# Kernel tuning notes

Measured on AMD Instinct MI355X. Metric: run time of the kernel, lower is better.

The kernel has to match this reference:

```python
import jax, jax.numpy as jnp
import numpy as np

NUM_HEADS = 8
Q_DIM = 32  # == k_dim == v_dim (required by the broadcasted matmul in the source)

def _conv1x1(x, w, b):
    # x: [B, C, H, W]; w: [O, C]; b: [O]  (1x1 conv == channel matmul)
    return jnp.einsum('bchw,oc->bohw', x, w) + b[None, :, None, None]

def setup_inputs() -> dict:
    key = jax.random.key(0)
    ks = jax.random.split(key, 7)
    B, C, H, W = 16, 256, 64, 64
    O = Q_DIM * NUM_HEADS  # 256
    s = 1.0 / np.sqrt(C)
    return {
        'x':  jax.random.normal(ks[0], (B, C, H, W), jnp.float32),
        'wq': jax.random.normal(ks[1], (O, C), jnp.float32) * s,
        'bq': jax.random.normal(ks[2], (O,), jnp.float32) * 0.01,
        'wk': jax.random.normal(ks[3], (O, C), jnp.float32) * s,
        'bk': jax.random.normal(ks[4], (O,), jnp.float32) * 0.01,
        'wv': jax.random.normal(ks[5], (O, C), jnp.float32) * s,
        'bv': jax.random.normal(ks[6], (O,), jnp.float32) * 0.01,
    }

def reference(x, wq, bq, wk, bk, wv, bv):
    B, C, H, W = x.shape
    nH, d = NUM_HEADS, Q_DIM
    q = _conv1x1(x, wq, bq).reshape(B, nH, d, H, W)
    k = _conv1x1(x, wk, bk).reshape(B, nH, d, H, W)
    v = _conv1x1(x, wv, bv).reshape(B, nH, d, H, W)
    # torch.matmul(q, k.transpose(-2,-1)): contract over width, batched over (B, nH, d)
    scores = jnp.einsum('bndhw,bndgw->bndhg', q, k) / jnp.sqrt(jnp.asarray(d, x.dtype))
    weights = jax.nn.softmax(scores, axis=-1)  # [B, nH, d, H, H]
    ctx = jnp.einsum('bndhg,bndgw->bndhw', weights, v)
    return ctx.reshape(B, nH * d, H, W)
```

## Files before the change

kernel.cpp:

```cpp
#include <hip/hip_runtime.h>
#include <stdint.h>

#define LOG2E       1.4426950408889634f
#define INV_SQRT32  0.17677669529663687f

using bf16x8 = __attribute__((ext_vector_type(8))) short;
using f32x4  = __attribute__((ext_vector_type(4))) float;

__device__ __forceinline__ unsigned short f2bf(float f) {
  union { float f; uint32_t u; } v; v.f = f;
  uint32_t r = v.u + 0x7fffu + ((v.u >> 16) & 1u);
  return (unsigned short)(r >> 16);
}

typedef const __attribute__((address_space(1))) void* gas_ptr;
typedef __attribute__((address_space(3))) void*       las_ptr;
__device__ __forceinline__ void load_lds16(const void* g, void* l) {
  __builtin_amdgcn_global_load_lds((gas_ptr)g, (las_ptr)l, 16, 0, 0);
}

__global__ __launch_bounds__(256) void convert_w(
    const float* __restrict__ wq, const float* __restrict__ bq,
    const float* __restrict__ wk, const float* __restrict__ bk,
    const float* __restrict__ wv, const float* __restrict__ bv,
    unsigned short* __restrict__ Wcat, float* __restrict__ biasc) {
  int idx = (blockIdx.x * 256 + threadIdx.x) * 4;
  int p = idx >> 16;
  int rem = idx & 0xffff;
  const float* src = (p == 0) ? wq : (p == 1) ? wk : wv;
  float4 v = *(const float4*)(src + rem);
  ushort4 o;
  o.x = f2bf(v.x); o.y = f2bf(v.y); o.z = f2bf(v.z); o.w = f2bf(v.w);
  *(ushort4*)(Wcat + idx) = o;
  if (blockIdx.x < 3) {
    const float* sb = (blockIdx.x == 0) ? bq : (blockIdx.x == 1) ? bk : bv;
    biasc[blockIdx.x * 256 + threadIdx.x] = sb[threadIdx.x];
  }
}

__global__ __launch_bounds__(256) void transpose_x(const float* __restrict__ x,
                                                   unsigned short* __restrict__ xt) {
  __shared__ float tile[64 * 65];
  int b = blockIdx.z;
  int s0 = blockIdx.x * 64, c0 = blockIdx.y * 64;
  int t = threadIdx.x;
  int sl = t & 63, g = t >> 6;
  const float* xp = x + ((size_t)(b * 256 + c0)) * 4096 + s0 + sl;
#pragma unroll
  for (int ii = 0; ii < 16; ++ii) {
    int cl = g * 16 + ii;
    tile[cl * 65 + sl] = xp[(size_t)cl * 4096];
  }
  __syncthreads();
#pragma unroll
  for (int it = 0; it < 2; ++it) {
    int idx = it * 256 + t;
    int s_loc = idx >> 3, cb = (idx & 7) * 8;
    unsigned short ov[8];
#pragma unroll
    for (int j = 0; j < 8; ++j) ov[j] = f2bf(tile[(cb + j) * 65 + s_loc]);
    *(uint4*)&xt[((size_t)(b * 4096 + s0 + s_loc)) * 256 + c0 + cb] = *(uint4*)ov;
  }
}

__global__ __launch_bounds__(256) void gemm_qkv(
    const unsigned short* __restrict__ Wc, const float* __restrict__ biasc,
    const unsigned short* __restrict__ Xt, unsigned short* __restrict__ qkv) {
  __shared__ unsigned short As[2][128 * 32];
  __shared__ unsigned short Bs[2][128 * 32];
  int blk = blockIdx.x;
  int b = blk / 192;
  int rest = blk - b * 192;
  int mt = rest >> 5, nt = rest & 31;
  int m0 = mt * 128, n0 = nt * 128;
  int tid = threadIdx.x;
  int lane = tid & 63, wave = tid >> 6;
  int quad = lane >> 4, rt = lane & 15;
  int wm = wave >> 1, wn = wave & 1;

  f32x4 acc[4][4];
#pragma unroll
  for (int i = 0; i < 4; ++i)
#pragma unroll
    for (int j = 0; j < 4; ++j) acc[i][j] = (f32x4){0.f, 0.f, 0.f, 0.f};

  int lr = lane >> 2;
  int sl_src = (lane & 3) ^ ((lane >> 3) & 3);
  const unsigned short* gA0 = Wc + (size_t)(m0 + wave * 32 + lr) * 256 + sl_src * 8;
  const unsigned short* gA1 = gA0 + 16 * 256;
  const unsigned short* gB0 = Xt + ((size_t)b * 4096 + n0 + wave * 32 + lr) * 256 + sl_src * 8;
  const unsigned short* gB1 = gB0 + 16 * 256;

#define STAGE(bufi, ko)                                        \
  do {                                                         \
    load_lds16(gA0 + (ko), &As[bufi][wave * 1024]);            \
    load_lds16(gA1 + (ko), &As[bufi][wave * 1024 + 512]);      \
    load_lds16(gB0 + (ko), &Bs[bufi][wave * 1024]);            \
    load_lds16(gB1 + (ko), &Bs[bufi][wave * 1024 + 512]);      \
  } while (0)

  int rsw = (quad ^ ((rt >> 1) & 3)) * 8;

  STAGE(0, 0);
  STAGE(1, 32);

#define KSTEP(kc, WAITN)                                                      \
  do {                                                                        \
    asm volatile("s_waitcnt vmcnt(" #WAITN ")" ::: "memory");                 \
    __builtin_amdgcn_s_barrier();                                             \
    __builtin_amdgcn_sched_barrier(0);                                        \
    const unsigned short* A_ = As[(kc) & 1];                                  \
    const unsigned short* B_ = Bs[(kc) & 1];                                  \
    bf16x8 af[4], bfr[4];                                                     \
    _Pragma("unroll")                                                         \
    for (int mi = 0; mi < 4; ++mi)                                            \
      af[mi] = *(const bf16x8*)&A_[(wm * 64 + mi * 16 + rt) * 32 + rsw];      \
    _Pragma("unroll")                                                         \
    for (int ni = 0; ni < 4; ++ni)                                            \
      bfr[ni] = *(const bf16x8*)&B_[(wn * 64 + ni * 16 + rt) * 32 + rsw];     \
    _Pragma("unroll")                                                         \
    for (int mi = 0; mi < 4; ++mi)                                            \
      _Pragma("unroll")                                                       \
      for (int ni = 0; ni < 4; ++ni)                                          \
        acc[mi][ni] = __builtin_amdgcn_mfma_f32_16x16x32_bf16(af[mi], bfr[ni], acc[mi][ni], 0, 0, 0); \
    __builtin_amdgcn_sched_barrier(0);                                        \
    __builtin_amdgcn_s_barrier();                                             \
    if ((kc) + 2 < 8) STAGE((kc) & 1, ((kc) + 2) * 32);                       \
  } while (0)

  KSTEP(0, 4);
  KSTEP(1, 4);
  KSTEP(2, 4);
  KSTEP(3, 4);
  KSTEP(4, 4);
  KSTEP(5, 4);
  KSTEP(6, 4);
  KSTEP(7, 0);
#undef KSTEP
#undef STAGE

  size_t obase = (size_t)b * 768;
#pragma unroll
  for (int mi = 0; mi < 4; ++mi) {
    int o = m0 + wm * 64 + mi * 16 + quad * 4;
    float bsv[4];
#pragma unroll
    for (int r = 0; r < 4; ++r) bsv[r] = biasc[o + r];
#pragma unroll
    for (int ni = 0; ni < 4; ++ni) {
      int s = n0 + wn * 64 + ni * 16 + rt;
#pragma unroll
      for (int r = 0; r < 4; ++r)
        qkv[(obase + o + r) * 4096 + s] = f2bf(acc[mi][ni][r] + bsv[r]);
    }
  }
}

__global__ __launch_bounds__(256) void attn(const unsigned short* __restrict__ qkv,
                                            float* __restrict__ out) {
  __shared__ char sh[36608];
  unsigned short* Qs = (unsigned short*)sh;
  unsigned short* Ks = (unsigned short*)(sh + 9216);
  float*          Sf = (float*)sh;
  unsigned short* Ps = (unsigned short*)(sh + 16640);
  unsigned short* Vt = (unsigned short*)(sh + 25856);
  float* red    = (float*)(sh + 35072);
  float* rowmax = (float*)(sh + 36096);
  float* rowinv = (float*)(sh + 36352);

  int blk = blockIdx.x;
  int b = blk >> 8, o = blk & 255;
  int t = threadIdx.x;
  size_t base = ((size_t)b * 768 + o) * 4096;
  const unsigned short* qg = qkv + base;
  const unsigned short* kg = qkv + base + (size_t)256 * 4096;
  const unsigned short* vg = qkv + base + (size_t)512 * 4096;

  {
    int h = t >> 2, w0 = (t & 3) * 16;
    const uint4* qp = (const uint4*)(qg + h * 64 + w0);
    const uint4* kp = (const uint4*)(kg + h * 64 + w0);
    uint4 q0 = qp[0], q1 = qp[1];
    uint4 k0 = kp[0], k1 = kp[1];
    *(uint4*)&Qs[h * 72 + w0]     = q0;
    *(uint4*)&Qs[h * 72 + w0 + 8] = q1;
    *(uint4*)&Ks[h * 72 + w0]     = k0;
    *(uint4*)&Ks[h * 72 + w0 + 8] = k1;

    int w = t & 63, gb = (t >> 6) * 16;
    unsigned short vv[16];
#pragma unroll
    for (int j = 0; j < 16; ++j) vv[j] = vg[(size_t)(gb + j) * 64 + w];
    *(uint4*)&Vt[w * 72 + gb]     = ((uint4*)vv)[0];
    *(uint4*)&Vt[w * 72 + gb + 8] = ((uint4*)vv)[1];
  }
  __syncthreads();

  int lane = t & 63, wave = t >> 6;
  int rt = lane & 15, quad = lane >> 4;
  int wm = wave >> 1, wn = wave & 1;

  f32x4 accs[2][2];
#pragma unroll
  for (int i = 0; i < 2; ++i)
#pragma unroll
    for (int j = 0; j < 2; ++j) accs[i][j] = (f32x4){0.f, 0.f, 0.f, 0.f};
#pragma unroll
  for (int ks = 0; ks < 2; ++ks) {
    int kk = ks * 32 + quad * 8;
    bf16x8 a0 = *(const bf16x8*)&Qs[(wm * 32 + rt) * 72 + kk];
    bf16x8 a1 = *(const bf16x8*)&Qs[(wm * 32 + 16 + rt) * 72 + kk];
    bf16x8 b0 = *(const bf16x8*)&Ks[(wn * 32 + rt) * 72 + kk];
    bf16x8 b1 = *(const bf16x8*)&Ks[(wn * 32 + 16 + rt) * 72 + kk];
    accs[0][0] = __builtin_amdgcn_mfma_f32_16x16x32_bf16(a0, b0, accs[0][0], 0, 0, 0);
    accs[0][1] = __builtin_amdgcn_mfma_f32_16x16x32_bf16(a0, b1, accs[0][1], 0, 0, 0);
    accs[1][0] = __builtin_amdgcn_mfma_f32_16x16x32_bf16(a1, b0, accs[1][0], 0, 0, 0);
    accs[1][1] = __builtin_amdgcn_mfma_f32_16x16x32_bf16(a1, b1, accs[1][1], 0, 0, 0);
  }
  __syncthreads();

#pragma unroll
  for (int tm = 0; tm < 2; ++tm)
#pragma unroll
    for (int tn = 0; tn < 2; ++tn)
#pragma unroll
      for (int r = 0; r < 4; ++r)
        Sf[(wm * 32 + tm * 16 + quad * 4 + r) * 65 + wn * 32 + tn * 16 + rt] =
            accs[tm][tn][r] * INV_SQRT32;
  __syncthreads();

  int hr = t & 63, qt = t >> 6;
  float s[16];
#pragma unroll
  for (int e = 0; e < 16; ++e) s[e] = Sf[hr * 65 + qt * 16 + e];
  float m = s[0];
#pragma unroll
  for (int e = 1; e < 16; ++e) m = fmaxf(m, s[e]);
  red[qt * 64 + hr] = m;
  __syncthreads();
  if (t < 64)
    rowmax[t] = fmaxf(fmaxf(red[t], red[64 + t]), fmaxf(red[128 + t], red[192 + t]));
  __syncthreads();
  float mr = rowmax[hr];
  float ssum = 0.f;
  unsigned short pv[16];
#pragma unroll
  for (int e = 0; e < 16; ++e) {
    float p = exp2f((s[e] - mr) * LOG2E);
    ssum += p;
    pv[e] = f2bf(p);
  }
  *(uint4*)&Ps[hr * 72 + qt * 16]     = ((uint4*)pv)[0];
  *(uint4*)&Ps[hr * 72 + qt * 16 + 8] = ((uint4*)pv)[1];
  red[qt * 64 + hr] = ssum;
  __syncthreads();
  if (t < 64) rowinv[t] = 1.f / (red[t] + red[64 + t] + red[128 + t] + red[192 + t]);
  __syncthreads();

  f32x4 acco[2][2];
#pragma unroll
  for (int i = 0; i < 2; ++i)
#pragma unroll
    for (int j = 0; j < 2; ++j) acco[i][j] = (f32x4){0.f, 0.f, 0.f, 0.f};
#pragma unroll
  for (int ks = 0; ks < 2; ++ks) {
    int kk = ks * 32 + quad * 8;
    bf16x8 a0 = *(const bf16x8*)&Ps[(wm * 32 + rt) * 72 + kk];
    bf16x8 a1 = *(const bf16x8*)&Ps[(wm * 32 + 16 + rt) * 72 + kk];
    bf16x8 b0 = *(const bf16x8*)&Vt[(wn * 32 + rt) * 72 + kk];
    bf16x8 b1 = *(const bf16x8*)&Vt[(wn * 32 + 16 + rt) * 72 + kk];
    acco[0][0] = __builtin_amdgcn_mfma_f32_16x16x32_bf16(a0, b0, acco[0][0], 0, 0, 0);
    acco[0][1] = __builtin_amdgcn_mfma_f32_16x16x32_bf16(a0, b1, acco[0][1], 0, 0, 0);
    acco[1][0] = __builtin_amdgcn_mfma_f32_16x16x32_bf16(a1, b0, acco[1][0], 0, 0, 0);
    acco[1][1] = __builtin_amdgcn_mfma_f32_16x16x32_bf16(a1, b1, acco[1][1], 0, 0, 0);
  }

  float* op = out + ((size_t)(b * 256 + o)) * 4096;
#pragma unroll
  for (int tm = 0; tm < 2; ++tm) {
#pragma unroll
    for (int r = 0; r < 4; ++r) {
      int h = wm * 32 + tm * 16 + quad * 4 + r;
      float inv = rowinv[h];
#pragma unroll
      for (int tn = 0; tn < 2; ++tn) {
        int w = wn * 32 + tn * 16 + rt;
        op[h * 64 + w] = acco[tm][tn][r] * inv;
      }
    }
  }
}

extern "C" void kernel_launch(void* const* d_in, const int* in_sizes, int n_in,
                              void* d_out, int out_size, void* d_ws, size_t ws_size,
                              hipStream_t stream) {
  const float* x  = (const float*)d_in[0];
  const float* wq = (const float*)d_in[1];
  const float* bq = (const float*)d_in[2];
  const float* wk = (const float*)d_in[3];
  const float* bk = (const float*)d_in[4];
  const float* wv = (const float*)d_in[5];
  const float* bv = (const float*)d_in[6];
  float* out = (float*)d_out;

  char* ws = (char*)d_ws;
  unsigned short* Wcat  = (unsigned short*)ws;
  float*          biasc = (float*)(ws + 393216);
  unsigned short* Xt    = (unsigned short*)(ws + 396288);
  unsigned short* qkv   = (unsigned short*)(ws + 396288 + 33554432);

  hipLaunchKernelGGL(convert_w, dim3(192), dim3(256), 0, stream,
                     wq, bq, wk, bk, wv, bv, Wcat, biasc);
  hipLaunchKernelGGL(transpose_x, dim3(64, 4, 16), dim3(256), 0, stream, x, Xt);
  hipLaunchKernelGGL(gemm_qkv, dim3(3072), dim3(256), 0, stream, Wcat, biasc, Xt, qkv);
  hipLaunchKernelGGL(attn, dim3(4096), dim3(256), 0, stream, qkv, out);
}
```

Baseline: 199.9 us.

## Triple-buffer GEMM, vectorize stores, register-level softmax in attention kernel

```diff
diff --git a/kernel.cpp b/kernel.cpp
--- a/kernel.cpp
+++ b/kernel.cpp
@@ -66,8 +66,8 @@
 __global__ __launch_bounds__(256) void gemm_qkv(
     const unsigned short* __restrict__ Wc, const float* __restrict__ biasc,
     const unsigned short* __restrict__ Xt, unsigned short* __restrict__ qkv) {
-  __shared__ unsigned short As[2][128 * 32];
-  __shared__ unsigned short Bs[2][128 * 32];
+  __shared__ unsigned short As[3][128 * 32];
+  __shared__ unsigned short Bs[3][128 * 32];
   int blk = blockIdx.x;
   int b = blk / 192;
   int rest = blk - b * 192;
@@ -103,14 +103,15 @@
 
   STAGE(0, 0);
   STAGE(1, 32);
+  STAGE(2, 64);
 
 #define KSTEP(kc, WAITN)                                                      \
   do {                                                                        \
     asm volatile("s_waitcnt vmcnt(" #WAITN ")" ::: "memory");                 \
     __builtin_amdgcn_s_barrier();                                             \
     __builtin_amdgcn_sched_barrier(0);                                        \
-    const unsigned short* A_ = As[(kc) & 1];                                  \
-    const unsigned short* B_ = Bs[(kc) & 1];                                  \
+    const unsigned short* A_ = As[(kc) % 3];                                  \
+    const unsigned short* B_ = Bs[(kc) % 3];                                  \
     bf16x8 af[4], bfr[4];                                                     \
     _Pragma("unroll")                                                         \
     for (int mi = 0; mi < 4; ++mi)                                            \
@@ -122,18 +123,18 @@
     for (int mi = 0; mi < 4; ++mi)                                            \
       _Pragma("unroll")                                                       \
       for (int ni = 0; ni < 4; ++ni)                                          \
-        acc[mi][ni] = __builtin_amdgcn_mfma_f32_16x16x32_bf16(af[mi], bfr[ni], acc[mi][ni], 0, 0, 0); \
+        acc[mi][ni] = __builtin_amdgcn_mfma_f32_16x16x32_bf16(bfr[ni], af[mi], acc[mi][ni], 0, 0, 0); \
     __builtin_amdgcn_sched_barrier(0);                                        \
     __builtin_amdgcn_s_barrier();                                             \
-    if ((kc) + 2 < 8) STAGE((kc) & 1, ((kc) + 2) * 32);                       \
+    if ((kc) + 3 < 8) STAGE((kc) % 3, ((kc) + 3) * 32);                       \
   } while (0)
 
-  KSTEP(0, 4);
-  KSTEP(1, 4);
-  KSTEP(2, 4);
-  KSTEP(3, 4);
-  KSTEP(4, 4);
-  KSTEP(5, 4);
+  KSTEP(0, 8);
+  KSTEP(1, 8);
+  KSTEP(2, 8);
+  KSTEP(3, 8);
+  KSTEP(4, 8);
+  KSTEP(5, 8);
   KSTEP(6, 4);
   KSTEP(7, 0);
 #undef KSTEP
@@ -142,31 +143,28 @@
   size_t obase = (size_t)b * 768;
 #pragma unroll
   for (int mi = 0; mi < 4; ++mi) {
-    int o = m0 + wm * 64 + mi * 16 + quad * 4;
-    float bsv[4];
-#pragma unroll
-    for (int r = 0; r < 4; ++r) bsv[r] = biasc[o + r];
+    int o = m0 + wm * 64 + mi * 16 + rt;
+    float bo = biasc[o];
+    size_t rowb = (obase + o) * 4096;
 #pragma unroll
     for (int ni = 0; ni < 4; ++ni) {
-      int s = n0 + wn * 64 + ni * 16 + rt;
-#pragma unroll
-      for (int r = 0; r < 4; ++r)
-        qkv[(obase + o + r) * 4096 + s] = f2bf(acc[mi][ni][r] + bsv[r]);
+      int s = n0 + wn * 64 + ni * 16 + quad * 4;
+      ushort4 st;
+      st.x = f2bf(acc[mi][ni][0] + bo);
+      st.y = f2bf(acc[mi][ni][1] + bo);
+      st.z = f2bf(acc[mi][ni][2] + bo);
+      st.w = f2bf(acc[mi][ni][3] + bo);
+      *(ushort4*)&qkv[rowb + s] = st;
     }
   }
 }
 
 __global__ __launch_bounds__(256) void attn(const unsigned short* __restrict__ qkv,
                                             float* __restrict__ out) {
-  __shared__ char sh[36608];
-  unsigned short* Qs = (unsigned short*)sh;
-  unsigned short* Ks = (unsigned short*)(sh + 9216);
-  float*          Sf = (float*)sh;
-  unsigned short* Ps = (unsigned short*)(sh + 16640);
-  unsigned short* Vt = (unsigned short*)(sh + 25856);
-  float* red    = (float*)(sh + 35072);
-  float* rowmax = (float*)(sh + 36096);
-  float* rowinv = (float*)(sh + 36352);
+  __shared__ unsigned short Vt[64 * 72];
+  __shared__ unsigned short Ps[64 * 72];
+  __shared__ float redm[128];
+  __shared__ float reds[128];
 
   int blk = blockIdx.x;
   int b = blk >> 8, o = blk & 255;
@@ -176,30 +174,15 @@
   const unsigned short* kg = qkv + base + (size_t)256 * 4096;
   const unsigned short* vg = qkv + base + (size_t)512 * 4096;
 
-  {
-    int h = t >> 2, w0 = (t & 3) * 16;
-    const uint4* qp = (const uint4*)(qg + h * 64 + w0);
-    const uint4* kp = (const uint4*)(kg + h * 64 + w0);
-    uint4 q0 = qp[0], q1 = qp[1];
-    uint4 k0 = kp[0], k1 = kp[1];
-    *(uint4*)&Qs[h * 72 + w0]     = q0;
-    *(uint4*)&Qs[h * 72 + w0 + 8] = q1;
-    *(uint4*)&Ks[h * 72 + w0]     = k0;
-    *(uint4*)&Ks[h * 72 + w0 + 8] = k1;
-
-    int w = t & 63, gb = (t >> 6) * 16;
-    unsigned short vv[16];
-#pragma unroll
-    for (int j = 0; j < 16; ++j) vv[j] = vg[(size_t)(gb + j) * 64 + w];
-    *(uint4*)&Vt[w * 72 + gb]     = ((uint4*)vv)[0];
-    *(uint4*)&Vt[w * 72 + gb + 8] = ((uint4*)vv)[1];
-  }
-  __syncthreads();
-
   int lane = t & 63, wave = t >> 6;
   int rt = lane & 15, quad = lane >> 4;
   int wm = wave >> 1, wn = wave & 1;
 
+  int vw = t & 63, gb = (t >> 6) * 16;
+  unsigned short vv[16];
+#pragma unroll
+  for (int j = 0; j < 16; ++j) vv[j] = vg[(size_t)(gb + j) * 64 + vw];
+
   f32x4 accs[2][2];
 #pragma unroll
   for (int i = 0; i < 2; ++i)
@@ -208,53 +191,82 @@
 #pragma unroll
   for (int ks = 0; ks < 2; ++ks) {
     int kk = ks * 32 + quad * 8;
-    bf16x8 a0 = *(const bf16x8*)&Qs[(wm * 32 + rt) * 72 + kk];
-    bf16x8 a1 = *(const bf16x8*)&Qs[(wm * 32 + 16 + rt) * 72 + kk];
-    bf16x8 b0 = *(const bf16x8*)&Ks[(wn * 32 + rt) * 72 + kk];
-    bf16x8 b1 = *(const bf16x8*)&Ks[(wn * 32 + 16 + rt) * 72 + kk];
+    bf16x8 a0 = *(const bf16x8*)&qg[(wm * 32 + rt) * 64 + kk];
+    bf16x8 a1 = *(const bf16x8*)&qg[(wm * 32 + 16 + rt) * 64 + kk];
+    bf16x8 b0 = *(const bf16x8*)&kg[(wn * 32 + rt) * 64 + kk];
+    bf16x8 b1 = *(const bf16x8*)&kg[(wn * 32 + 16 + rt) * 64 + kk];
     accs[0][0] = __builtin_amdgcn_mfma_f32_16x16x32_bf16(a0, b0, accs[0][0], 0, 0, 0);
     accs[0][1] = __builtin_amdgcn_mfma_f32_16x16x32_bf16(a0, b1, accs[0][1], 0, 0, 0);
     accs[1][0] = __builtin_amdgcn_mfma_f32_16x16x32_bf16(a1, b0, accs[1][0], 0, 0, 0);
     accs[1][1] = __builtin_amdgcn_mfma_f32_16x16x32_bf16(a1, b1, accs[1][1], 0, 0, 0);
   }
+
+  float sv[2][2][4];
+#pragma unroll
+  for (int tm = 0; tm < 2; ++tm)
+#pragma unroll
+    for (int tn = 0; tn < 2; ++tn)
+#pragma unroll
+      for (int r = 0; r < 4; ++r) sv[tm][tn][r] = accs[tm][tn][r] * INV_SQRT32;
+
+  float pmax[2][4];
+#pragma unroll
+  for (int tm = 0; tm < 2; ++tm)
+#pragma unroll
+    for (int r = 0; r < 4; ++r) {
+      float m = fmaxf(sv[tm][0][r], sv[tm][1][r]);
+      m = fmaxf(m, __shfl_xor(m, 1));
+      m = fmaxf(m, __shfl_xor(m, 2));
+      m = fmaxf(m, __shfl_xor(m, 4));
+      m = fmaxf(m, __shfl_xor(m, 8));
+      pmax[tm][r] = m;
+    }
+  if (rt == 0) {
+#pragma unroll
+    for (int tm = 0; tm < 2; ++tm)
+#pragma unroll
+      for (int r = 0; r < 4; ++r)
+        redm[wn * 64 + wm * 32 + tm * 16 + quad * 4 + r] = pmax[tm][r];
+  }
   __syncthreads();
 
+  float psum[2][4];
+  unsigned short pb[2][2][4];
 #pragma unroll
   for (int tm = 0; tm < 2; ++tm)
 #pragma unroll
+    for (int r = 0; r < 4; ++r) {
+      int h = wm * 32 + tm * 16 + quad * 4 + r;
+      float mr = fmaxf(redm[h], redm[64 + h]);
+      float acc_s = 0.f;
+#pragma unroll
+      for (int tn = 0; tn < 2; ++tn) {
+        float p = exp2f((sv[tm][tn][r] - mr) * LOG2E);
+        acc_s += p;
+        pb[tm][tn][r] = f2bf(p);
+      }
+      acc_s += __shfl_xor(acc_s, 1);
+      acc_s += __shfl_xor(acc_s, 2);
+      acc_s += __shfl_xor(acc_s, 4);
+      acc_s += __shfl_xor(acc_s, 8);
+      psum[tm][r] = acc_s;
+    }
+  if (rt == 0) {
+#pragma unroll
+    for (int tm = 0; tm < 2; ++tm)
+#pragma unroll
+      for (int r = 0; r < 4; ++r)
+        reds[wn * 64 + wm * 32 + tm * 16 + quad * 4 + r] = psum[tm][r];
+  }
+#pragma unroll
+  for (int tm = 0; tm < 2; ++tm)
+#pragma unroll
     for (int tn = 0; tn < 2; ++tn)
 #pragma unroll
       for (int r = 0; r < 4; ++r)
-        Sf[(wm * 32 + tm * 16 + quad * 4 + r) * 65 + wn * 32 + tn * 16 + rt] =
-            accs[tm][tn][r] * INV_SQRT32;
-  __syncthreads();
-
-  int hr = t & 63, qt = t >> 6;
-  float s[16];
-#pragma unroll
-  for (int e = 0; e < 16; ++e) s[e] = Sf[hr * 65 + qt * 16 + e];
-  float m = s[0];
-#pragma unroll
-  for (int e = 1; e < 16; ++e) m = fmaxf(m, s[e]);
-  red[qt * 64 + hr] = m;
-  __syncthreads();
-  if (t < 64)
-    rowmax[t] = fmaxf(fmaxf(red[t], red[64 + t]), fmaxf(red[128 + t], red[192 + t]));
-  __syncthreads();
-  float mr = rowmax[hr];
-  float ssum = 0.f;
-  unsigned short pv[16];
-#pragma unroll
-  for (int e = 0; e < 16; ++e) {
-    float p = exp2f((s[e] - mr) * LOG2E);
-    ssum += p;
-    pv[e] = f2bf(p);
-  }
-  *(uint4*)&Ps[hr * 72 + qt * 16]     = ((uint4*)pv)[0];
-  *(uint4*)&Ps[hr * 72 + qt * 16 + 8] = ((uint4*)pv)[1];
-  red[qt * 64 + hr] = ssum;
-  __syncthreads();
-  if (t < 64) rowinv[t] = 1.f / (red[t] + red[64 + t] + red[128 + t] + red[192 + t]);
+        Ps[(wm * 32 + tm * 16 + quad * 4 + r) * 72 + wn * 32 + tn * 16 + rt] = pb[tm][tn][r];
+  *(uint4*)&Vt[vw * 72 + gb]     = ((uint4*)vv)[0];
+  *(uint4*)&Vt[vw * 72 + gb + 8] = ((uint4*)vv)[1];
   __syncthreads();
 
   f32x4 acco[2][2];
@@ -265,28 +277,30 @@
 #pragma unroll
   for (int ks = 0; ks < 2; ++ks) {
     int kk = ks * 32 + quad * 8;
-    bf16x8 a0 = *(const bf16x8*)&Ps[(wm * 32 + rt) * 72 + kk];
-    bf16x8 a1 = *(const bf16x8*)&Ps[(wm * 32 + 16 + rt) * 72 + kk];
-    bf16x8 b0 = *(const bf16x8*)&Vt[(wn * 32 + rt) * 72 + kk];
-    bf16x8 b1 = *(const bf16x8*)&Vt[(wn * 32 + 16 + rt) * 72 + kk];
-    acco[0][0] = __builtin_amdgcn_mfma_f32_16x16x32_bf16(a0, b0, acco[0][0], 0, 0, 0);
-    acco[0][1] = __builtin_amdgcn_mfma_f32_16x16x32_bf16(a0, b1, acco[0][1], 0, 0, 0);
-    acco[1][0] = __builtin_amdgcn_mfma_f32_16x16x32_bf16(a1, b0, acco[1][0], 0, 0, 0);
-    acco[1][1] = __builtin_amdgcn_mfma_f32_16x16x32_bf16(a1, b1, acco[1][1], 0, 0, 0);
+    bf16x8 va0 = *(const bf16x8*)&Vt[(wm * 32 + rt) * 72 + kk];
+    bf16x8 va1 = *(const bf16x8*)&Vt[(wm * 32 + 16 + rt) * 72 + kk];
+    bf16x8 p0  = *(const bf16x8*)&Ps[(wn * 32 + rt) * 72 + kk];
+    bf16x8 p1  = *(const bf16x8*)&Ps[(wn * 32 + 16 + rt) * 72 + kk];
+    acco[0][0] = __builtin_amdgcn_mfma_f32_16x16x32_bf16(va0, p0, acco[0][0], 0, 0, 0);
+    acco[0][1] = __builtin_amdgcn_mfma_f32_16x16x32_bf16(va0, p1, acco[0][1], 0, 0, 0);
+    acco[1][0] = __builtin_amdgcn_mfma_f32_16x16x32_bf16(va1, p0, acco[1][0], 0, 0, 0);
+    acco[1][1] = __builtin_amdgcn_mfma_f32_16x16x32_bf16(va1, p1, acco[1][1], 0, 0, 0);
   }
 
   float* op = out + ((size_t)(b * 256 + o)) * 4096;
 #pragma unroll
-  for (int tm = 0; tm < 2; ++tm) {
-#pragma unroll
-    for (int r = 0; r < 4; ++r) {
-      int h = wm * 32 + tm * 16 + quad * 4 + r;
-      float inv = rowinv[h];
-#pragma unroll
-      for (int tn = 0; tn < 2; ++tn) {
-        int w = wn * 32 + tn * 16 + rt;
-        op[h * 64 + w] = acco[tm][tn][r] * inv;
-      }
+  for (int hi = 0; hi < 2; ++hi) {
+    int h = wn * 32 + hi * 16 + rt;
+    float rinv = 1.f / (reds[h] + reds[64 + h]);
+#pragma unroll
+    for (int wi = 0; wi < 2; ++wi) {
+      int w0 = wm * 32 + wi * 16 + quad * 4;
+      float4 st;
+      st.x = acco[wi][hi][0] * rinv;
+      st.y = acco[wi][hi][1] * rinv;
+      st.z = acco[wi][hi][2] * rinv;
+      st.w = acco[wi][hi][3] * rinv;
+      *(float4*)&op[h * 64 + w0] = st;
     }
   }
 }
```

Result: slower. 216.0 us (+8.0%).
